# Kernel tuning notes

Measured on AMD Instinct MI355X. Metric: run time of the kernel, lower is better.

## Reference

```python
import jax, jax.numpy as jnp
import numpy as np

N_NODES = 50000
N_EDGES = 800000
D_IN = 64
D_OUT = 64


def setup_inputs() -> dict:
    key = jax.random.key(0)
    k1, k2, k3, k4, k5, k6 = jax.random.split(key, 6)
    feat = jax.random.normal(k1, (N_NODES, D_IN), dtype=jnp.float32)
    edge_weight = jax.random.uniform(k2, (N_EDGES, 1), dtype=jnp.float32)
    # xavier_uniform bound for [D_IN, D_OUT]
    bound = float(np.sqrt(6.0 / (D_IN + D_OUT)))
    W1 = jax.random.uniform(k3, (D_IN, D_OUT), minval=-bound, maxval=bound, dtype=jnp.float32)
    W2 = jax.random.uniform(k4, (D_IN, D_OUT), minval=-bound, maxval=bound, dtype=jnp.float32)
    src = jax.random.randint(k5, (N_EDGES,), 0, N_NODES, dtype=jnp.int64)
    dst = jax.random.randint(k6, (N_EDGES,), 0, N_NODES, dtype=jnp.int64)
    return {"feat": feat, "edge_weight": edge_weight, "W1": W1, "W2": W2, "src": src, "dst": dst}


def reference(feat, edge_weight, W1, W2, src, dst):
    # message: u_sub_e -> src feature minus (broadcast) edge weight  [E, D_IN]
    msgs = feat[src] - edge_weight
    # sum aggregation over destination nodes  [N, D_IN]
    agg = jax.ops.segment_sum(msgs, dst, num_segments=feat.shape[0])
    # dual dense projections; no activation (activation=None)
    rst = jnp.matmul(feat, W1) + jnp.matmul(agg, W2)
    return rst
```

## Files before the change

kernel.cpp:

```cpp
#include <hip/hip_runtime.h>

#define NN 50000
#define NE 800000
#define D  64
#define NB 782
#define EBLK 2048
#define NEB 391
#define CAPB 1280

typedef unsigned int u32;
typedef unsigned short u16;
typedef unsigned long long u64;
typedef __attribute__((ext_vector_type(8))) short bf16x8;
typedef __attribute__((ext_vector_type(4))) float f32x4;
typedef __attribute__((ext_vector_type(2))) float f32x2;

__device__ __forceinline__ int wave_incl_scan(int v, int lane) {
    #pragma unroll
    for (int off = 1; off < 64; off <<= 1) {
        int t = __shfl_up(v, off);
        if (lane >= off) v += t;
    }
    return v;
}

__device__ __forceinline__ u32 f2bf(float x) {
    u32 u = __float_as_uint(x);
    return (u + 0x7fffu + ((u >> 16) & 1u)) >> 16;
}

__device__ __forceinline__ bf16x8 as_bf8(uint4 u) {
    union { uint4 a; bf16x8 b; } x; x.a = u; return x.b;
}

__device__ __forceinline__ u32 pk_fp8x4(float a, float b, float c, float d) {
    int w = __builtin_amdgcn_cvt_pk_fp8_f32(a, b, 0, false);
    w = __builtin_amdgcn_cvt_pk_fp8_f32(c, d, w, true);
    return (u32)w;
}

__device__ __forceinline__ uint2 fp8x4_to_bf16x4(u32 uu) {
    f32x2 lo = __builtin_amdgcn_cvt_pk_f32_fp8((int)uu, false);
    f32x2 hi = __builtin_amdgcn_cvt_pk_f32_fp8((int)uu, true);
    uint2 r;
    r.x = f2bf(lo.x) | (f2bf(lo.y) << 16);
    r.y = f2bf(hi.x) | (f2bf(hi.y) << 16);
    return r;
}

__global__ __launch_bounds__(1024) void kb_scatter(const int* __restrict__ src,
                                                   const int* __restrict__ dst,
                                                   const float* __restrict__ ew,
                                                   const float* __restrict__ feat,
                                                   u32* __restrict__ cursor,
                                                   u64* __restrict__ sorted,
                                                   uint2* __restrict__ featb8)
{
    __shared__ u32 h[NB], eb[NB], ctr[NB], gb[NB];
    __shared__ u32 cTot[16], cOff[16];
    __shared__ u64 buf[EBLK];
    const int tid  = threadIdx.x;
    const int w    = tid >> 6;
    const int lane = tid & 63;

    for (int i = tid; i < NB; i += 1024) h[i] = 0;
    __syncthreads();
    int base = blockIdx.x * EBLK;
    int n = min(EBLK, NE - base);

    u32 rd[2], rs[2], rw[2];
    #pragma unroll
    for (int j = 0; j < 2; ++j) {
        int k = tid + j * 1024;
        if (k < n) {
            int e = base + k;
            rd[j] = (u32)dst[e];
            rs[j] = (u32)src[e];
            rw[j] = __float_as_uint(ew[e]);
            atomicAdd(&h[rd[j] >> 6], 1u);
        }
    }
    __syncthreads();
    if (w < 13) {
        int idx = w * 64 + lane;
        u32 v = (idx < NB) ? h[idx] : 0;
        int incl = wave_incl_scan((int)v, lane);
        if (idx < NB) eb[idx] = (u32)incl - v;
        if (lane == 63) cTot[w] = (u32)incl;
    }
    __syncthreads();
    if (w == 0) {
        u32 v = (lane < 13) ? cTot[lane] : 0;
        int incl = wave_incl_scan((int)v, lane);
        if (lane < 16) cOff[lane] = (u32)incl - v;
    }
    __syncthreads();
    for (int i = tid; i < NB; i += 1024) {
        u32 e = eb[i] + cOff[i >> 6];
        eb[i] = e; ctr[i] = e;
        gb[i] = atomicAdd(&cursor[i], h[i]);
    }
    __syncthreads();
    #pragma unroll
    for (int j = 0; j < 2; ++j) {
        int k = tid + j * 1024;
        if (k < n) {
            u64 rec = ((u64)((rd[j] << 16) | rs[j]) << 32) | (u64)rw[j];
            u32 p = atomicAdd(&ctr[rd[j] >> 6], 1u);
            buf[p] = rec;
        }
    }
    __syncthreads();
    for (int k = tid; k < n; k += 1024) {
        u64 rec = buf[k];
        u32 bin = (u32)(rec >> 54);
        u32 idx = gb[bin] + (u32)k - eb[bin];
        if (idx < CAPB) sorted[(size_t)bin * CAPB + idx] = rec;
    }

    {
        int i = blockIdx.x * 1024 + tid;
        if (i < NN * D / 8) {
            const float4* f4 = (const float4*)feat;
            float4 a = f4[2 * i], b = f4[2 * i + 1];
            uint2 p8;
            p8.x = pk_fp8x4(a.x, a.y, a.z, a.w);
            p8.y = pk_fp8x4(b.x, b.y, b.z, b.w);
            featb8[i] = p8;
        }
    }
}

__global__ __launch_bounds__(1024) void kcgg(
    const u64* __restrict__ sorted,
    const u32* __restrict__ cursor,
    const u32* __restrict__ fb8,
    const float* __restrict__ W1,
    const float* __restrict__ W2,
    float* __restrict__ out)
{
    __shared__ u32 hcnt[64], hbase[65], ctr[64];
    __shared__ u16 bufS[CAPB];
    __shared__ u32 bufWf[CAPB];
    __shared__ u16 aggT[64][72];
    __shared__ u16 wT[64][136];
    __shared__ float csp[4][64];
    __shared__ float csum[64];
    __shared__ float sWs[64];

    const int tid = threadIdx.x;
    const int bin = blockIdx.x;
    const int n = min((int)cursor[bin], CAPB);
    const size_t rbase = (size_t)bin * CAPB;

    for (int i = tid; i < 8192; i += 1024) {
        int k = i >> 6, c = i & 63;
        float v = (k < 64) ? W1[i] : W2[i - 4096];
        wT[c][k] = (u16)f2bf(v);
    }
    if (tid < 256) {
        int c = tid & 63, kq = tid >> 6;
        float s = 0.f;
        for (int k = kq * 16; k < kq * 16 + 16; ++k) s += W2[k * 64 + c];
        csp[kq][c] = s;
    }
    if (tid < 64) hcnt[tid] = 0;
    __syncthreads();
    if (tid < 64) csum[tid] = csp[0][tid] + csp[1][tid] + csp[2][tid] + csp[3][tid];
    for (int k = tid; k < n; k += 1024)
        atomicAdd(&hcnt[(int)(sorted[rbase + k] >> 48) & 63], 1u);
    __syncthreads();
    if (tid < 64) {
        u32 v = hcnt[tid];
        int incl = wave_incl_scan((int)v, tid);
        u32 ex = (u32)incl - v;
        hbase[tid] = ex; ctr[tid] = ex;
        if (tid == 63) hbase[64] = (u32)incl;
    }
    __syncthreads();
    for (int k = tid; k < n; k += 1024) {
        u64 rec = sorted[rbase + k];
        u32 p = atomicAdd(&ctr[(int)(rec >> 48) & 63], 1u);
        bufS[p]  = (u16)(rec >> 32);
        bufWf[p] = (u32)rec;
    }
    __syncthreads();

    const int w    = tid >> 6;
    const int lane = tid & 63;
    const int g    = lane >> 4;
    const int li   = lane & 15;
    const int ln   = w * 4 + g;

    int e   = (int)hbase[ln];
    int end = (int)hbase[ln + 1];

    if (li == 0) {
        float s = 0.f;
        for (int j = e; j < end; ++j) s += __uint_as_float(bufWf[j]);
        sWs[ln] = s;
    }

    float4 acc = make_float4(0.f, 0.f, 0.f, 0.f);
    for (; e + 7 < end; e += 8) {
        int s0 = bufS[e],     s1 = bufS[e + 1];
        int s2 = bufS[e + 2], s3 = bufS[e + 3];
        int s4 = bufS[e + 4], s5 = bufS[e + 5];
        int s6 = bufS[e + 6], s7 = bufS[e + 7];
        u32 u0 = fb8[(size_t)s0 * 16 + li];
        u32 u1 = fb8[(size_t)s1 * 16 + li];
        u32 u2 = fb8[(size_t)s2 * 16 + li];
        u32 u3 = fb8[(size_t)s3 * 16 + li];
        u32 u4 = fb8[(size_t)s4 * 16 + li];
        u32 u5 = fb8[(size_t)s5 * 16 + li];
        u32 u6 = fb8[(size_t)s6 * 16 + li];
        u32 u7 = fb8[(size_t)s7 * 16 + li];
        #pragma unroll
        for (int j = 0; j < 8; ++j) {
            u32 uu = j == 0 ? u0 : j == 1 ? u1 : j == 2 ? u2 : j == 3 ? u3
                   : j == 4 ? u4 : j == 5 ? u5 : j == 6 ? u6 : u7;
            f32x2 lo = __builtin_amdgcn_cvt_pk_f32_fp8((int)uu, false);
            f32x2 hi = __builtin_amdgcn_cvt_pk_f32_fp8((int)uu, true);
            acc.x += lo.x; acc.y += lo.y; acc.z += hi.x; acc.w += hi.y;
        }
    }
    for (; e < end; ++e) {
        u32 uu = fb8[(size_t)bufS[e] * 16 + li];
        f32x2 lo = __builtin_amdgcn_cvt_pk_f32_fp8((int)uu, false);
        f32x2 hi = __builtin_amdgcn_cvt_pk_f32_fp8((int)uu, true);
        acc.x += lo.x; acc.y += lo.y; acc.z += hi.x; acc.w += hi.y;
    }
    {
        uint2 o;
        o.x = f2bf(acc.x) | (f2bf(acc.y) << 16);
        o.y = f2bf(acc.z) | (f2bf(acc.w) << 16);
        *(uint2*)&aggT[ln][li * 4] = o;
    }
    __syncthreads();

    const int nt = w >> 2;
    const int ct = w & 3;
    const int lr = lane & 15;
    const int q  = lane >> 4;
    const int m0 = (bin << 6) + nt * 16;

    bf16x8 b0 = *(const bf16x8*)&wT[ct * 16 + lr][ 0 + q * 8];
    bf16x8 b1 = *(const bf16x8*)&wT[ct * 16 + lr][32 + q * 8];
    bf16x8 b2 = *(const bf16x8*)&wT[ct * 16 + lr][64 + q * 8];
    bf16x8 b3 = *(const bf16x8*)&wT[ct * 16 + lr][96 + q * 8];

    const size_t arow = (size_t)(m0 + lr) * 16;
    u32 f0 = fb8[arow + q * 2], f1 = fb8[arow + q * 2 + 1];
    u32 f2 = fb8[arow + 8 + q * 2], f3 = fb8[arow + 8 + q * 2 + 1];
    uint2 r0 = fp8x4_to_bf16x4(f0), r1 = fp8x4_to_bf16x4(f1);
    uint2 r2 = fp8x4_to_bf16x4(f2), r3 = fp8x4_to_bf16x4(f3);
    bf16x8 a0 = as_bf8(make_uint4(r0.x, r0.y, r1.x, r1.y));
    bf16x8 a1 = as_bf8(make_uint4(r2.x, r2.y, r3.x, r3.y));
    bf16x8 a2 = *(const bf16x8*)&aggT[nt * 16 + lr][q * 8];
    bf16x8 a3 = *(const bf16x8*)&aggT[nt * 16 + lr][32 + q * 8];

    f32x4 o4 = {0.f, 0.f, 0.f, 0.f};
    o4 = __builtin_amdgcn_mfma_f32_16x16x32_bf16(a0, b0, o4, 0, 0, 0);
    o4 = __builtin_amdgcn_mfma_f32_16x16x32_bf16(a1, b1, o4, 0, 0, 0);
    o4 = __builtin_amdgcn_mfma_f32_16x16x32_bf16(a2, b2, o4, 0, 0, 0);
    o4 = __builtin_amdgcn_mfma_f32_16x16x32_bf16(a3, b3, o4, 0, 0, 0);

    #pragma unroll
    for (int r = 0; r < 4; ++r) {
        int row = m0 + q * 4 + r;
        if (row < NN) {
            float s = sWs[nt * 16 + q * 4 + r];
            out[(size_t)row * D + ct * 16 + lr] = o4[r] - s * csum[ct * 16 + lr];
        }
    }
}

extern "C" void kernel_launch(void* const* d_in, const int* in_sizes, int n_in,
                              void* d_out, int out_size, void* d_ws, size_t ws_size,
                              hipStream_t stream)
{
    const float* feat = (const float*)d_in[0];
    const float* ew   = (const float*)d_in[1];
    const float* W1   = (const float*)d_in[2];
    const float* W2   = (const float*)d_in[3];
    const int*   src  = (const int*)  d_in[4];
    const int*   dst  = (const int*)  d_in[5];
    float* out = (float*)d_out;

    char* p = (char*)d_ws;
    size_t o = 0;
    auto take = [&](size_t bytes) { char* q = p + o; o = (o + bytes + 255) & ~(size_t)255; return q; };
    u64* sorted   = (u64*)take((size_t)NB * CAPB * 8);
    u32* cursor   = (u32*)take((size_t)NB * 4);
    uint2* featb8 = (uint2*)take((size_t)NN * D + 4096);

    hipMemsetAsync(cursor, 0, (size_t)NB * 4, stream);
    kb_scatter<<<NEB, 1024, 0, stream>>>(src, dst, ew, feat, cursor, sorted,
                                         (uint2*)featb8);
    kcgg      <<<NB, 1024, 0, stream>>>(sorted, cursor, (const u32*)featb8,
                                        W1, W2, out);
}
```

Measured before the change: 52.75 us.

## Balance gather work by splitting block edges evenly across groups with atomic LDS accumulation

Each 16-lane group used to own one destination node and process all of its edges, so groups with high-degree nodes set the pace. Now the block's edge list is split into 64 equal ranges. Each group binary-searches for its starting node, walks runs that cross node boundaries, and flushes its partial sums with float atomics into an fp32 LDS aggregation buffer. This removes load imbalance across degree variation, at the cost of LDS zeroing, shared-memory atomics, a smaller unroll and an extra fp32-to-bf16 conversion before the MFMA.

```diff
diff --git a/kernel.cpp b/kernel.cpp
--- a/kernel.cpp
+++ b/kernel.cpp
@@ -142,7 +142,7 @@
     __shared__ u32 hcnt[64], hbase[65], ctr[64];
     __shared__ u16 bufS[CAPB];
     __shared__ u32 bufWf[CAPB];
-    __shared__ u16 aggT[64][72];
+    __shared__ float aggF[64][68];
     __shared__ u16 wT[64][136];
     __shared__ float csp[4][64];
     __shared__ float csum[64];
@@ -158,13 +158,14 @@
         float v = (k < 64) ? W1[i] : W2[i - 4096];
         wT[c][k] = (u16)f2bf(v);
     }
+    for (int i = tid; i < 64 * 68; i += 1024) ((float*)aggF)[i] = 0.f;
     if (tid < 256) {
         int c = tid & 63, kq = tid >> 6;
         float s = 0.f;
         for (int k = kq * 16; k < kq * 16 + 16; ++k) s += W2[k * 64 + c];
         csp[kq][c] = s;
     }
-    if (tid < 64) hcnt[tid] = 0;
+    if (tid < 64) { hcnt[tid] = 0; sWs[tid] = 0.f; }
     __syncthreads();
     if (tid < 64) csum[tid] = csp[0][tid] + csp[1][tid] + csp[2][tid] + csp[3][tid];
     for (int k = tid; k < n; k += 1024)
@@ -190,51 +191,59 @@
     const int lane = tid & 63;
     const int g    = lane >> 4;
     const int li   = lane & 15;
-    const int ln   = w * 4 + g;
-
-    int e   = (int)hbase[ln];
-    int end = (int)hbase[ln + 1];
-
-    if (li == 0) {
-        float s = 0.f;
-        for (int j = e; j < end; ++j) s += __uint_as_float(bufWf[j]);
-        sWs[ln] = s;
-    }
-
-    float4 acc = make_float4(0.f, 0.f, 0.f, 0.f);
-    for (; e + 7 < end; e += 8) {
-        int s0 = bufS[e],     s1 = bufS[e + 1];
-        int s2 = bufS[e + 2], s3 = bufS[e + 3];
-        int s4 = bufS[e + 4], s5 = bufS[e + 5];
-        int s6 = bufS[e + 6], s7 = bufS[e + 7];
-        u32 u0 = fb8[(size_t)s0 * 16 + li];
-        u32 u1 = fb8[(size_t)s1 * 16 + li];
-        u32 u2 = fb8[(size_t)s2 * 16 + li];
-        u32 u3 = fb8[(size_t)s3 * 16 + li];
-        u32 u4 = fb8[(size_t)s4 * 16 + li];
-        u32 u5 = fb8[(size_t)s5 * 16 + li];
-        u32 u6 = fb8[(size_t)s6 * 16 + li];
-        u32 u7 = fb8[(size_t)s7 * 16 + li];
-        #pragma unroll
-        for (int j = 0; j < 8; ++j) {
-            u32 uu = j == 0 ? u0 : j == 1 ? u1 : j == 2 ? u2 : j == 3 ? u3
-                   : j == 4 ? u4 : j == 5 ? u5 : j == 6 ? u6 : u7;
-            f32x2 lo = __builtin_amdgcn_cvt_pk_f32_fp8((int)uu, false);
-            f32x2 hi = __builtin_amdgcn_cvt_pk_f32_fp8((int)uu, true);
-            acc.x += lo.x; acc.y += lo.y; acc.z += hi.x; acc.w += hi.y;
-        }
-    }
-    for (; e < end; ++e) {
-        u32 uu = fb8[(size_t)bufS[e] * 16 + li];
-        f32x2 lo = __builtin_amdgcn_cvt_pk_f32_fp8((int)uu, false);
-        f32x2 hi = __builtin_amdgcn_cvt_pk_f32_fp8((int)uu, true);
-        acc.x += lo.x; acc.y += lo.y; acc.z += hi.x; acc.w += hi.y;
-    }
+    const int gid  = w * 4 + g;
+
     {
-        uint2 o;
-        o.x = f2bf(acc.x) | (f2bf(acc.y) << 16);
-        o.y = f2bf(acc.z) | (f2bf(acc.w) << 16);
-        *(uint2*)&aggT[ln][li * 4] = o;
+        int lo = (gid * n) >> 6;
+        int hi = ((gid + 1) * n) >> 6;
+        int ln = 0;
+        {
+            int l = 0, r = 64;
+            while (l < r) {
+                int m = (l + r + 1) >> 1;
+                if ((int)hbase[m] <= lo) l = m; else r = m - 1;
+            }
+            ln = l;
+        }
+        int e = lo;
+        int nb = (int)hbase[ln + 1];
+        while (e < hi) {
+            int runEnd = min(hi, nb);
+            float4 acc = make_float4(0.f, 0.f, 0.f, 0.f);
+            float ws = 0.f;
+            for (; e + 3 < runEnd; e += 4) {
+                int s0 = bufS[e],     s1 = bufS[e + 1];
+                int s2 = bufS[e + 2], s3 = bufS[e + 3];
+                u32 u0 = fb8[(size_t)s0 * 16 + li];
+                u32 u1 = fb8[(size_t)s1 * 16 + li];
+                u32 u2 = fb8[(size_t)s2 * 16 + li];
+                u32 u3 = fb8[(size_t)s3 * 16 + li];
+                if (li == 0)
+                    ws += __uint_as_float(bufWf[e]) + __uint_as_float(bufWf[e + 1])
+                        + __uint_as_float(bufWf[e + 2]) + __uint_as_float(bufWf[e + 3]);
+                #pragma unroll
+                for (int j = 0; j < 4; ++j) {
+                    u32 uu = j == 0 ? u0 : j == 1 ? u1 : j == 2 ? u2 : u3;
+                    f32x2 lo2 = __builtin_amdgcn_cvt_pk_f32_fp8((int)uu, false);
+                    f32x2 hi2 = __builtin_amdgcn_cvt_pk_f32_fp8((int)uu, true);
+                    acc.x += lo2.x; acc.y += lo2.y; acc.z += hi2.x; acc.w += hi2.y;
+                }
+            }
+            for (; e < runEnd; ++e) {
+                u32 uu = fb8[(size_t)bufS[e] * 16 + li];
+                if (li == 0) ws += __uint_as_float(bufWf[e]);
+                f32x2 lo2 = __builtin_amdgcn_cvt_pk_f32_fp8((int)uu, false);
+                f32x2 hi2 = __builtin_amdgcn_cvt_pk_f32_fp8((int)uu, true);
+                acc.x += lo2.x; acc.y += lo2.y; acc.z += hi2.x; acc.w += hi2.y;
+            }
+            atomicAdd(&aggF[ln][li * 4 + 0], acc.x);
+            atomicAdd(&aggF[ln][li * 4 + 1], acc.y);
+            atomicAdd(&aggF[ln][li * 4 + 2], acc.z);
+            atomicAdd(&aggF[ln][li * 4 + 3], acc.w);
+            if (li == 0) atomicAdd(&sWs[ln], ws);
+            if (e >= hi) break;
+            do { ++ln; nb = (int)hbase[ln + 1]; } while (nb <= e);
+        }
     }
     __syncthreads();
 
@@ -256,8 +265,19 @@
     uint2 r2 = fp8x4_to_bf16x4(f2), r3 = fp8x4_to_bf16x4(f3);
     bf16x8 a0 = as_bf8(make_uint4(r0.x, r0.y, r1.x, r1.y));
     bf16x8 a1 = as_bf8(make_uint4(r2.x, r2.y, r3.x, r3.y));
-    bf16x8 a2 = *(const bf16x8*)&aggT[nt * 16 + lr][q * 8];
-    bf16x8 a3 = *(const bf16x8*)&aggT[nt * 16 + lr][32 + q * 8];
+
+    const float* ar = &aggF[nt * 16 + lr][0];
+    uint4 a2u, a3u;
+    a2u.x = f2bf(ar[q * 8 + 0]) | (f2bf(ar[q * 8 + 1]) << 16);
+    a2u.y = f2bf(ar[q * 8 + 2]) | (f2bf(ar[q * 8 + 3]) << 16);
+    a2u.z = f2bf(ar[q * 8 + 4]) | (f2bf(ar[q * 8 + 5]) << 16);
+    a2u.w = f2bf(ar[q * 8 + 6]) | (f2bf(ar[q * 8 + 7]) << 16);
+    a3u.x = f2bf(ar[32 + q * 8 + 0]) | (f2bf(ar[32 + q * 8 + 1]) << 16);
+    a3u.y = f2bf(ar[32 + q * 8 + 2]) | (f2bf(ar[32 + q * 8 + 3]) << 16);
+    a3u.z = f2bf(ar[32 + q * 8 + 4]) | (f2bf(ar[32 + q * 8 + 5]) << 16);
+    a3u.w = f2bf(ar[32 + q * 8 + 6]) | (f2bf(ar[32 + q * 8 + 7]) << 16);
+    bf16x8 a2 = as_bf8(a2u);
+    bf16x8 a3 = as_bf8(a3u);
 
     f32x4 o4 = {0.f, 0.f, 0.f, 0.f};
     o4 = __builtin_amdgcn_mfma_f32_16x16x32_bf16(a0, b0, o4, 0, 0, 0);
```

Result: slower. 90.55 us (+71.7%).
